# Kernel tuning notes

Measured on AMD Instinct MI355X. Metric: run time of the kernel, lower is better.

Reference implementation:

```python
import jax, jax.numpy as jnp
import numpy as np

B, R, S, D = 8, 128, 512, 33      # batch, ref (grid), seq_len, input_dim (enc_in*2+1)
E, H = 128, 4                     # embed_time, num_heads
EK = E // H                       # per-head dim
NH = 128                          # nhidden
NEG = -1e9


def setup_inputs() -> dict:
    key = jax.random.key(0)
    ks = jax.random.split(key, 16)
    inp = {
        'query': jax.random.normal(ks[0], (B, R, E), jnp.float32),
        'key':   jax.random.normal(ks[1], (B, S, E), jnp.float32),
        'value': jax.random.normal(ks[2], (B, S, D), jnp.float32),
        'mask':  (jax.random.uniform(ks[3], (B, S, D)) < 0.7).astype(jnp.float32),
        'qt':    jnp.sort(jax.random.uniform(ks[4], (R,), jnp.float32)),
        'tt':    jax.random.uniform(ks[5], (B, S), jnp.float32),
        'stride': 0.1 * jax.random.normal(ks[6], (D,), jnp.float32),
        # learned params (torch Linear layout: W [out, in])
        'Wq': jax.random.normal(ks[7], (E, E), jnp.float32) / np.sqrt(E),
        'bq': jnp.zeros((E,), jnp.float32),
        'Wk': jax.random.normal(ks[8], (E, E), jnp.float32) / np.sqrt(E),
        'bk': jnp.zeros((E,), jnp.float32),
        'Wr': jax.random.normal(ks[9], (D, D), jnp.float32) / np.sqrt(D),
        'br': jnp.zeros((D,), jnp.float32),
        'Wo': jax.random.normal(ks[10], (NH, H * D), jnp.float32) / np.sqrt(H * D),
        'bo': jnp.zeros((NH,), jnp.float32),
    }
    return inp


def reference(query, key, value, mask, qt, tt, stride, Wq, bq, Wk, bk, Wr, br, Wo, bo):
    b, r, _ = query.shape
    s = key.shape[1]
    d = value.shape[-1]
    # stride gate: sigmoid(Linear(D,D)(stride))  -> [D]
    sa = jax.nn.sigmoid(stride @ Wr.T + br)
    # projections, split heads: [B,H,R,EK] / [B,H,S,EK]
    q = (query @ Wq.T + bq).reshape(b, r, H, EK).transpose(0, 2, 1, 3)
    k = (key @ Wk.T + bk).reshape(b, s, H, EK).transpose(0, 2, 1, 3)
    # scores: [B,H,R,S]
    scores = jnp.einsum('bhre,bhse->bhrs', q, k) / np.sqrt(EK)
    # per-query time window mask, vectorized over the 'ref' loop: [B,R,S,D]
    t = tt[:, None, :, None]                      # [B,1,S,1]
    qtb = qt[None, :, None, None]                 # [1,R,1,1]
    win = (t <= qtb + sa) & (t >= qtb - sa)       # [B,R,S,D] (sa broadcasts on D)
    allm = win & (mask[:, None, :, :] != 0)       # [B,R,S,D]
    # broadcast scores over value dim D, mask, softmax over seq axis (dim=-2)
    sc = jnp.where(allm[:, None], scores[..., None], NEG)  # [B,H,R,S,D]
    p = jax.nn.softmax(sc, axis=-2)
    # masked weighted sum over seq: [B,H,R,D]
    x = jnp.einsum('bhrsd,bsd->bhrd', p, value)
    x = x.transpose(0, 2, 1, 3).reshape(b, r, H * d)
    out = x @ Wo.T + bo                           # [B,R,NH]
    return out, sa
```

## Files before the change

kernel.cpp:

```cpp
#include <hip/hip_runtime.h>

#define BB   8
#define RR   128
#define SS   512
#define DD   33
#define EE   128
#define HH   4
#define EKK  32
#define NHH  128
#define HD   (HH*DD)

#define WS_QP   0
#define WS_KT   (BB*RR*EE)
#define WS_WOT  (WS_KT + BB*EE*SS)

#define NB_KP   512
#define NB_QP2  128
#define NB_WOT2 66
#define NB_PREP (NB_KP + NB_QP2 + NB_WOT2)

__global__ __launch_bounds__(256) void prep_kernel(
    const float* __restrict__ query, const float* __restrict__ key,
    const float* __restrict__ Wq, const float* __restrict__ bq,
    const float* __restrict__ Wk, const float* __restrict__ bk,
    const float* __restrict__ Wo, float* __restrict__ ws)
{
    __shared__ float rows[8 * EE];
    int blk = blockIdx.x, tid = threadIdx.x;

    if (blk < NB_KP) {
        int s8 = blk * 8;
#pragma unroll
        for (int i = 0; i < 4; ++i) rows[i * 256 + tid] = key[s8 * EE + i * 256 + tid];
        __syncthreads();
        int g = tid >> 7, e = tid & 127;
        float acc[4];
        float bv = bk[e];
#pragma unroll
        for (int p = 0; p < 4; ++p) acc[p] = bv;
        const float4* W4 = (const float4*)(Wk + e * EE);
        const float4* R4 = (const float4*)rows;
#pragma unroll
        for (int j = 0; j < EE / 4; ++j) {
            float4 w = W4[j];
#pragma unroll
            for (int p = 0; p < 4; ++p) {
                float4 rv = R4[(g * 4 + p) * 32 + j];
                acc[p] += w.x * rv.x + w.y * rv.y + w.z * rv.z + w.w * rv.w;
            }
        }
        int b = s8 / SS, s0 = s8 % SS;
        float4 v; v.x = acc[0]; v.y = acc[1]; v.z = acc[2]; v.w = acc[3];
        *(float4*)(ws + WS_KT + (b * EE + e) * SS + s0 + g * 4) = v;
        return;
    }
    blk -= NB_KP;

    if (blk < NB_QP2) {
        int br0 = blk * 8;
#pragma unroll
        for (int i = 0; i < 4; ++i) rows[i * 256 + tid] = query[br0 * EE + i * 256 + tid];
        __syncthreads();
        int g = tid >> 7, e = tid & 127;
        float acc[4];
        float bv = bq[e];
#pragma unroll
        for (int p = 0; p < 4; ++p) acc[p] = bv;
        const float4* W4 = (const float4*)(Wq + e * EE);
        const float4* R4 = (const float4*)rows;
#pragma unroll
        for (int j = 0; j < EE / 4; ++j) {
            float4 w = W4[j];
#pragma unroll
            for (int p = 0; p < 4; ++p) {
                float4 rv = R4[(g * 4 + p) * 32 + j];
                acc[p] += w.x * rv.x + w.y * rv.y + w.z * rv.z + w.w * rv.w;
            }
        }
#pragma unroll
        for (int p = 0; p < 4; ++p)
            ws[WS_QP + (br0 + g * 4 + p) * EE + e] = acc[p];
        return;
    }
    blk -= NB_QP2;

    {
        int gid = blk * 256 + tid;
        if (gid < HD * NHH) {
            int n = gid & 127, j = gid >> 7;
            ws[WS_WOT + gid] = Wo[n * HD + j];
        }
    }
}

#define POOL_REDP 0
#define POOL_REDW 2048
#define POOL_REDV 4096
#define POOL_R32P 4352
#define POOL_R32W 4416
#define POOL_R32V 4480
#define EIDX(rr,h,s) (((rr)*HH+(h))*SS + (s))

__global__ __launch_bounds__(512) void fused_kernel(
    const float* __restrict__ qp, const float* __restrict__ kt,
    const float* __restrict__ value, const float* __restrict__ maskp,
    const float* __restrict__ tt, const float* __restrict__ qt,
    const float* __restrict__ stridev, const float* __restrict__ Wr,
    const float* __restrict__ brv, const float* __restrict__ wot,
    const float* __restrict__ bo, float* __restrict__ out)
{
    __shared__ float s_q[2][EE];
    __shared__ float s_tt[SS];
    __shared__ float s_sa[DD + 3];
    __shared__ float s_pool[4488];
    __shared__ float s_x[2][HD];
    __shared__ float s_part[4][NHH];

    int blk = blockIdx.x;
    int b  = blk >> 6;
    int r0 = (blk & 63) * 2;
    int tid = threadIdx.x;

    if (tid < 256) s_q[tid >> 7][tid & 127] =
        qp[(b * RR + r0 + (tid >> 7)) * EE + (tid & 127)];
    s_tt[tid] = tt[b * SS + tid];
    if (tid < DD) {
        float acc = brv[tid];
#pragma unroll
        for (int j = 0; j < DD; ++j) acc += stridev[j] * Wr[tid * DD + j];
        float sv = 1.0f / (1.0f + __expf(-acc));
        s_sa[tid] = sv;
        if (blk == 0) out[BB * RR * NHH + tid] = sv;
    }
    __syncthreads();

    {
        int h = tid >> 7, sq = tid & 127;
        const float* kb = kt + (b * EE + h * EKK) * SS;
        float4 a0 = {0,0,0,0}, a1 = {0,0,0,0};
#pragma unroll
        for (int e = 0; e < EKK; ++e) {
            float4 kv = ((const float4*)(kb + e * SS))[sq];
            float q0 = s_q[0][h * EKK + e];
            float q1 = s_q[1][h * EKK + e];
            a0.x += q0 * kv.x; a0.y += q0 * kv.y; a0.z += q0 * kv.z; a0.w += q0 * kv.w;
            a1.x += q1 * kv.x; a1.y += q1 * kv.y; a1.z += q1 * kv.z; a1.w += q1 * kv.w;
        }
        const float scale = 0.17677669529663687f;
        float4 e0, e1;
        e0.x = __expf(a0.x * scale); e0.y = __expf(a0.y * scale);
        e0.z = __expf(a0.z * scale); e0.w = __expf(a0.w * scale);
        e1.x = __expf(a1.x * scale); e1.y = __expf(a1.y * scale);
        e1.z = __expf(a1.z * scale); e1.w = __expf(a1.w * scale);
        ((float4*)&s_pool[EIDX(0, h, 0)])[sq] = e0;
        ((float4*)&s_pool[EIDX(1, h, 0)])[sq] = e1;
    }
    __syncthreads();

    int wv = tid >> 6, lane = tid & 63;
    int sp = lane >> 5, d = lane & 31;
    int s0 = wv * 64;
    float qtr0 = qt[r0], qtr1 = qt[r0 + 1];

    float ps0[HH] = {0,0,0,0}, ps1[HH] = {0,0,0,0};
    float ws0_[HH] = {0,0,0,0}, ws1_[HH] = {0,0,0,0};
    float vsum = 0.f;
    {
        float sad = s_sa[d];
        float lo0 = qtr0 - sad, hi0 = qtr0 + sad;
        float lo1 = qtr1 - sad, hi1 = qtr1 + sad;
        const float* vp = value + (size_t)(b * SS + s0 + sp) * DD + d;
        const float* mp = maskp + (size_t)(b * SS + s0 + sp) * DD + d;
#pragma unroll 4
        for (int i = 0; i < 32; ++i) {
            int s = s0 + 2 * i + sp;
            float vv = vp[i * 2 * DD];
            float mv = mp[i * 2 * DD];
            float tv = s_tt[s];
            bool mb = (mv != 0.f);
            bool k0 = mb & (tv >= lo0) & (tv <= hi0);
            bool k1 = mb & (tv >= lo1) & (tv <= hi1);
            vsum += vv;
#pragma unroll
            for (int h = 0; h < HH; ++h) {
                float e0 = s_pool[EIDX(0, h, s)];
                float e1 = s_pool[EIDX(1, h, s)];
                float p0 = k0 ? e0 : 0.f;
                float p1 = k1 ? e1 : 0.f;
                ps0[h] += p0; ws0_[h] += p0 * vv;
                ps1[h] += p1; ws1_[h] += p1 * vv;
            }
        }
#pragma unroll
        for (int h = 0; h < HH; ++h) {
            ps0[h] += __shfl_xor(ps0[h], 32); ws0_[h] += __shfl_xor(ws0_[h], 32);
            ps1[h] += __shfl_xor(ps1[h], 32); ws1_[h] += __shfl_xor(ws1_[h], 32);
        }
        vsum += __shfl_xor(vsum, 32);
    }

    float tps = 0.f, tws = 0.f, tvs = 0.f;
    {
        int trr = lane >> 5, th = (lane >> 3) & 3, tj = lane & 7;
        float sad = s_sa[32];
        float lo = (trr ? qtr1 : qtr0) - sad, hi = (trr ? qtr1 : qtr0) + sad;
#pragma unroll
        for (int i = 0; i < 8; ++i) {
            int s = s0 + tj * 8 + i;
            float vv = value[(size_t)(b * SS + s) * DD + 32];
            float mv = maskp[(size_t)(b * SS + s) * DD + 32];
            float tv = s_tt[s];
            bool k = (mv != 0.f) & (tv >= lo) & (tv <= hi);
            float e = s_pool[EIDX(trr, th, s)];
            float p = k ? e : 0.f;
            tps += p; tws += p * vv; tvs += vv;
        }
#pragma unroll
        for (int off = 1; off < 8; off <<= 1) {
            tps += __shfl_xor(tps, off);
            tws += __shfl_xor(tws, off);
            tvs += __shfl_xor(tvs, off);
        }
    }
    __syncthreads();

    if (lane < 32) {
#pragma unroll
        for (int h = 0; h < HH; ++h) {
            s_pool[POOL_REDP + ((wv * 2 + 0) * HH + h) * 32 + lane] = ps0[h];
            s_pool[POOL_REDP + ((wv * 2 + 1) * HH + h) * 32 + lane] = ps1[h];
            s_pool[POOL_REDW + ((wv * 2 + 0) * HH + h) * 32 + lane] = ws0_[h];
            s_pool[POOL_REDW + ((wv * 2 + 1) * HH + h) * 32 + lane] = ws1_[h];
        }
        s_pool[POOL_REDV + wv * 32 + lane] = vsum;
    }
    if ((lane & 7) == 0) {
        int trr = lane >> 5, th = (lane >> 3) & 3;
        s_pool[POOL_R32P + (wv * 2 + trr) * HH + th] = tps;
        s_pool[POOL_R32W + (wv * 2 + trr) * HH + th] = tws;
        if (lane == 0) s_pool[POOL_R32V + wv] = tvs;
    }
    __syncthreads();

    if (tid < 256) {
        int rr = tid >> 7, hd = tid & 127, h = hd >> 5, dd = hd & 31;
        float p = 0.f, w = 0.f;
#pragma unroll
        for (int k = 0; k < 8; ++k) {
            p += s_pool[POOL_REDP + ((k * 2 + rr) * HH + h) * 32 + dd];
            w += s_pool[POOL_REDW + ((k * 2 + rr) * HH + h) * 32 + dd];
        }
        float xv;
        if (p > 0.f) xv = w / p;
        else {
            float va = 0.f;
#pragma unroll
            for (int k = 0; k < 8; ++k) va += s_pool[POOL_REDV + k * 32 + dd];
            xv = va * (1.0f / SS);
        }
        s_x[rr][h * DD + dd] = xv;
    } else if (tid < 264) {
        int t = tid - 256, rr = t >> 2, h = t & 3;
        float p = 0.f, w = 0.f;
#pragma unroll
        for (int k = 0; k < 8; ++k) {
            p += s_pool[POOL_R32P + (k * 2 + rr) * HH + h];
            w += s_pool[POOL_R32W + (k * 2 + rr) * HH + h];
        }
        float xv;
        if (p > 0.f) xv = w / p;
        else {
            float va = 0.f;
#pragma unroll
            for (int k = 0; k < 8; ++k) va += s_pool[POOL_R32V + k];
            xv = va * (1.0f / SS);
        }
        s_x[rr][h * DD + 32] = xv;
    }
    __syncthreads();

    {
        int g2 = tid >> 7;
        int rr = g2 >> 1, jg = g2 & 1;
        int n = tid & 127;
        float acc = 0.f;
#pragma unroll
        for (int j = 0; j < 66; ++j)
            acc += s_x[rr][jg * 66 + j] * wot[(jg * 66 + j) * NHH + n];
        s_part[g2][n] = acc;
    }
    __syncthreads();
    if (tid < 256) {
        int rr = tid >> 7, n = tid & 127;
        out[(b * RR + r0 + rr) * NHH + n] =
            bo[n] + s_part[rr * 2][n] + s_part[rr * 2 + 1][n];
    }
}

extern "C" void kernel_launch(void* const* d_in, const int* in_sizes, int n_in,
                              void* d_out, int out_size, void* d_ws, size_t ws_size,
                              hipStream_t stream) {
    const float* query   = (const float*)d_in[0];
    const float* key     = (const float*)d_in[1];
    const float* value   = (const float*)d_in[2];
    const float* mask    = (const float*)d_in[3];
    const float* qt      = (const float*)d_in[4];
    const float* tt      = (const float*)d_in[5];
    const float* stridev = (const float*)d_in[6];
    const float* Wq      = (const float*)d_in[7];
    const float* bq      = (const float*)d_in[8];
    const float* Wk      = (const float*)d_in[9];
    const float* bk      = (const float*)d_in[10];
    const float* Wr      = (const float*)d_in[11];
    const float* brv     = (const float*)d_in[12];
    const float* Wo      = (const float*)d_in[13];
    const float* bo      = (const float*)d_in[14];

    float* out = (float*)d_out;
    float* ws  = (float*)d_ws;

    prep_kernel<<<NB_PREP, 256, 0, stream>>>(
        query, key, Wq, bq, Wk, bk, Wo, ws);
    fused_kernel<<<BB * 64, 512, 0, stream>>>(
        ws + WS_QP, ws + WS_KT, value, mask, tt, qt,
        stridev, Wr, brv, ws + WS_WOT, bo, out);
}
```

Before: 39.89 us.

## Merge prep and attention kernels into one cooperative kernel with grid sync

Folds the key projection, query projection and Wo transpose into the main attention kernel and separates them from the attention phase with a cooperative grid-wide barrier, falling back to the two-kernel path when co-residency is not possible. The query projection is now computed per block directly into shared memory instead of round-tripping through the workspace. The aim is to remove the second launch and the gap between kernels. In exchange it adds grid-sync cost, host-side occupancy queries on every call, and a co-residency requirement for 512 blocks of 512 threads.

Result: no change. 39.79 us (-0.2%).

```diff
diff --git a/kernel.cpp b/kernel.cpp
--- a/kernel.cpp
+++ b/kernel.cpp
@@ -1,4 +1,7 @@
 #include <hip/hip_runtime.h>
+#include <hip/hip_cooperative_groups.h>
+
+namespace cg = cooperative_groups;
 
 #define BB   8
 #define RR   128
@@ -10,88 +13,9 @@
 #define NHH  128
 #define HD   (HH*DD)
 
-#define WS_QP   0
-#define WS_KT   (BB*RR*EE)
-#define WS_WOT  (WS_KT + BB*EE*SS)
-
-#define NB_KP   512
-#define NB_QP2  128
-#define NB_WOT2 66
-#define NB_PREP (NB_KP + NB_QP2 + NB_WOT2)
-
-__global__ __launch_bounds__(256) void prep_kernel(
-    const float* __restrict__ query, const float* __restrict__ key,
-    const float* __restrict__ Wq, const float* __restrict__ bq,
-    const float* __restrict__ Wk, const float* __restrict__ bk,
-    const float* __restrict__ Wo, float* __restrict__ ws)
-{
-    __shared__ float rows[8 * EE];
-    int blk = blockIdx.x, tid = threadIdx.x;
-
-    if (blk < NB_KP) {
-        int s8 = blk * 8;
-#pragma unroll
-        for (int i = 0; i < 4; ++i) rows[i * 256 + tid] = key[s8 * EE + i * 256 + tid];
-        __syncthreads();
-        int g = tid >> 7, e = tid & 127;
-        float acc[4];
-        float bv = bk[e];
-#pragma unroll
-        for (int p = 0; p < 4; ++p) acc[p] = bv;
-        const float4* W4 = (const float4*)(Wk + e * EE);
-        const float4* R4 = (const float4*)rows;
-#pragma unroll
-        for (int j = 0; j < EE / 4; ++j) {
-            float4 w = W4[j];
-#pragma unroll
-            for (int p = 0; p < 4; ++p) {
-                float4 rv = R4[(g * 4 + p) * 32 + j];
-                acc[p] += w.x * rv.x + w.y * rv.y + w.z * rv.z + w.w * rv.w;
-            }
-        }
-        int b = s8 / SS, s0 = s8 % SS;
-        float4 v; v.x = acc[0]; v.y = acc[1]; v.z = acc[2]; v.w = acc[3];
-        *(float4*)(ws + WS_KT + (b * EE + e) * SS + s0 + g * 4) = v;
-        return;
-    }
-    blk -= NB_KP;
-
-    if (blk < NB_QP2) {
-        int br0 = blk * 8;
-#pragma unroll
-        for (int i = 0; i < 4; ++i) rows[i * 256 + tid] = query[br0 * EE + i * 256 + tid];
-        __syncthreads();
-        int g = tid >> 7, e = tid & 127;
-        float acc[4];
-        float bv = bq[e];
-#pragma unroll
-        for (int p = 0; p < 4; ++p) acc[p] = bv;
-        const float4* W4 = (const float4*)(Wq + e * EE);
-        const float4* R4 = (const float4*)rows;
-#pragma unroll
-        for (int j = 0; j < EE / 4; ++j) {
-            float4 w = W4[j];
-#pragma unroll
-            for (int p = 0; p < 4; ++p) {
-                float4 rv = R4[(g * 4 + p) * 32 + j];
-                acc[p] += w.x * rv.x + w.y * rv.y + w.z * rv.z + w.w * rv.w;
-            }
-        }
-#pragma unroll
-        for (int p = 0; p < 4; ++p)
-            ws[WS_QP + (br0 + g * 4 + p) * EE + e] = acc[p];
-        return;
-    }
-    blk -= NB_QP2;
-
-    {
-        int gid = blk * 256 + tid;
-        if (gid < HD * NHH) {
-            int n = gid & 127, j = gid >> 7;
-            ws[WS_WOT + gid] = Wo[n * HD + j];
-        }
-    }
-}
+#define WS_KT   0
+#define WS_WOT  (BB*EE*SS)
+#define WS_QP   (WS_WOT + HD*NHH)
 
 #define POOL_REDP 0
 #define POOL_REDW 2048
@@ -101,13 +25,16 @@
 #define POOL_R32V 4480
 #define EIDX(rr,h,s) (((rr)*HH+(h))*SS + (s))
 
-__global__ __launch_bounds__(512) void fused_kernel(
-    const float* __restrict__ qp, const float* __restrict__ kt,
+__global__ __launch_bounds__(512, 4) void mega_kernel(
+    const float* __restrict__ query, const float* __restrict__ key,
     const float* __restrict__ value, const float* __restrict__ maskp,
-    const float* __restrict__ tt, const float* __restrict__ qt,
-    const float* __restrict__ stridev, const float* __restrict__ Wr,
-    const float* __restrict__ brv, const float* __restrict__ wot,
-    const float* __restrict__ bo, float* __restrict__ out)
+    const float* __restrict__ qt, const float* __restrict__ tt,
+    const float* __restrict__ stridev,
+    const float* __restrict__ Wq, const float* __restrict__ bq,
+    const float* __restrict__ Wk, const float* __restrict__ bk,
+    const float* __restrict__ Wr, const float* __restrict__ brv,
+    const float* __restrict__ Wo, const float* __restrict__ bo,
+    float* __restrict__ ws, float* __restrict__ out)
 {
     __shared__ float s_q[2][EE];
     __shared__ float s_tt[SS];
@@ -115,14 +42,15 @@
     __shared__ float s_pool[4488];
     __shared__ float s_x[2][HD];
     __shared__ float s_part[4][NHH];
-
-    int blk = blockIdx.x;
-    int b  = blk >> 6;
-    int r0 = (blk & 63) * 2;
-    int tid = threadIdx.x;
-
-    if (tid < 256) s_q[tid >> 7][tid & 127] =
-        qp[(b * RR + r0 + (tid >> 7)) * EE + (tid & 127)];
+    __shared__ float s_rows[8 * EE];
+
+    int bid = blockIdx.x, tid = threadIdx.x;
+    int b  = bid >> 6;
+    int r0 = (bid & 63) * 2;
+
+    int s8 = bid * 8;
+    s_rows[tid]       = key[s8 * EE + tid];
+    s_rows[tid + 512] = key[s8 * EE + 512 + tid];
     s_tt[tid] = tt[b * SS + tid];
     if (tid < DD) {
         float acc = brv[tid];
@@ -130,9 +58,55 @@
         for (int j = 0; j < DD; ++j) acc += stridev[j] * Wr[tid * DD + j];
         float sv = 1.0f / (1.0f + __expf(-acc));
         s_sa[tid] = sv;
-        if (blk == 0) out[BB * RR * NHH + tid] = sv;
-    }
-    __syncthreads();
+        if (bid == 0) out[BB * RR * NHH + tid] = sv;
+    }
+    if (bid < 66) {
+        int gid = bid * 256 + tid;
+        if (gid < HD * NHH) {
+            int n = gid & 127, j = gid >> 7;
+            ws[WS_WOT + gid] = Wo[n * HD + j];
+        }
+    }
+    __syncthreads();
+
+    {
+        int g = tid >> 7, e = tid & 127;
+        float acc0 = bk[e], acc1 = acc0;
+        const float4* W4 = (const float4*)(Wk + e * EE);
+        const float4* R4 = (const float4*)s_rows;
+#pragma unroll
+        for (int j = 0; j < EE / 4; ++j) {
+            float4 w  = W4[j];
+            float4 r0v = R4[(g * 2 + 0) * 32 + j];
+            float4 r1v = R4[(g * 2 + 1) * 32 + j];
+            acc0 += w.x * r0v.x + w.y * r0v.y + w.z * r0v.z + w.w * r0v.w;
+            acc1 += w.x * r1v.x + w.y * r1v.y + w.z * r1v.z + w.w * r1v.w;
+        }
+        int kb = s8 / SS, s0 = s8 % SS;
+        float2 v; v.x = acc0; v.y = acc1;
+        *(float2*)(ws + WS_KT + (kb * EE + e) * SS + s0 + g * 2) = v;
+    }
+    __syncthreads();
+
+    if (tid < 256) s_rows[tid] = query[(b * RR + r0 + (tid >> 7)) * EE + (tid & 127)];
+    __syncthreads();
+    if (tid < 256) {
+        int rr = tid >> 7, e = tid & 127;
+        float acc = bq[e];
+        const float4* W4 = (const float4*)(Wq + e * EE);
+        const float4* R4 = (const float4*)(s_rows + rr * EE);
+#pragma unroll
+        for (int j = 0; j < EE / 4; ++j) {
+            float4 w = W4[j]; float4 rv = R4[j];
+            acc += w.x * rv.x + w.y * rv.y + w.z * rv.z + w.w * rv.w;
+        }
+        s_q[rr][e] = acc;
+    }
+
+    cg::this_grid().sync();
+
+    const float* kt  = ws + WS_KT;
+    const float* wot = ws + WS_WOT;
 
     {
         int h = tid >> 7, sq = tid & 127;
@@ -297,13 +271,288 @@
     }
 }
 
+#define NB_KP   512
+#define NB_QP2  128
+#define NB_WOT2 66
+#define NB_PREP (NB_KP + NB_QP2 + NB_WOT2)
+
+__global__ __launch_bounds__(256) void prep_kernel(
+    const float* __restrict__ query, const float* __restrict__ key,
+    const float* __restrict__ Wq, const float* __restrict__ bq,
+    const float* __restrict__ Wk, const float* __restrict__ bk,
+    const float* __restrict__ Wo, float* __restrict__ ws)
+{
+    __shared__ float rows[8 * EE];
+    int blk = blockIdx.x, tid = threadIdx.x;
+
+    if (blk < NB_KP) {
+        int s8 = blk * 8;
+#pragma unroll
+        for (int i = 0; i < 4; ++i) rows[i * 256 + tid] = key[s8 * EE + i * 256 + tid];
+        __syncthreads();
+        int g = tid >> 7, e = tid & 127;
+        float acc[4];
+        float bv = bk[e];
+#pragma unroll
+        for (int p = 0; p < 4; ++p) acc[p] = bv;
+        const float4* W4 = (const float4*)(Wk + e * EE);
+        const float4* R4 = (const float4*)rows;
+#pragma unroll
+        for (int j = 0; j < EE / 4; ++j) {
+            float4 w = W4[j];
+#pragma unroll
+            for (int p = 0; p < 4; ++p) {
+                float4 rv = R4[(g * 4 + p) * 32 + j];
+                acc[p] += w.x * rv.x + w.y * rv.y + w.z * rv.z + w.w * rv.w;
+            }
+        }
+        int b = s8 / SS, s0 = s8 % SS;
+        float4 v; v.x = acc[0]; v.y = acc[1]; v.z = acc[2]; v.w = acc[3];
+        *(float4*)(ws + WS_KT + (b * EE + e) * SS + s0 + g * 4) = v;
+        return;
+    }
+    blk -= NB_KP;
+
+    if (blk < NB_QP2) {
+        int br0 = blk * 8;
+#pragma unroll
+        for (int i = 0; i < 4; ++i) rows[i * 256 + tid] = query[br0 * EE + i * 256 + tid];
+        __syncthreads();
+        int g = tid >> 7, e = tid & 127;
+        float acc[4];
+        float bv = bq[e];
+#pragma unroll
+        for (int p = 0; p < 4; ++p) acc[p] = bv;
+        const float4* W4 = (const float4*)(Wq + e * EE);
+        const float4* R4 = (const float4*)rows;
+#pragma unroll
+        for (int j = 0; j < EE / 4; ++j) {
+            float4 w = W4[j];
+#pragma unroll
+            for (int p = 0; p < 4; ++p) {
+                float4 rv = R4[(g * 4 + p) * 32 + j];
+                acc[p] += w.x * rv.x + w.y * rv.y + w.z * rv.z + w.w * rv.w;
+            }
+        }
+#pragma unroll
+        for (int p = 0; p < 4; ++p)
+            ws[WS_QP + (br0 + g * 4 + p) * EE + e] = acc[p];
+        return;
+    }
+    blk -= NB_QP2;
+
+    {
+        int gid = blk * 256 + tid;
+        if (gid < HD * NHH) {
+            int n = gid & 127, j = gid >> 7;
+            ws[WS_WOT + gid] = Wo[n * HD + j];
+        }
+    }
+}
+
+__global__ __launch_bounds__(512) void fused_kernel(
+    const float* __restrict__ qp, const float* __restrict__ kt,
+    const float* __restrict__ value, const float* __restrict__ maskp,
+    const float* __restrict__ tt, const float* __restrict__ qt,
+    const float* __restrict__ stridev, const float* __restrict__ Wr,
+    const float* __restrict__ brv, const float* __restrict__ wot,
+    const float* __restrict__ bo, float* __restrict__ out)
+{
+    __shared__ float s_q[2][EE];
+    __shared__ float s_tt[SS];
+    __shared__ float s_sa[DD + 3];
+    __shared__ float s_pool[4488];
+    __shared__ float s_x[2][HD];
+    __shared__ float s_part[4][NHH];
+
+    int blk = blockIdx.x;
+    int b  = blk >> 6;
+    int r0 = (blk & 63) * 2;
+    int tid = threadIdx.x;
+
+    if (tid < 256) s_q[tid >> 7][tid & 127] =
+        qp[(b * RR + r0 + (tid >> 7)) * EE + (tid & 127)];
+    s_tt[tid] = tt[b * SS + tid];
+    if (tid < DD) {
+        float acc = brv[tid];
+#pragma unroll
+        for (int j = 0; j < DD; ++j) acc += stridev[j] * Wr[tid * DD + j];
+        float sv = 1.0f / (1.0f + __expf(-acc));
+        s_sa[tid] = sv;
+        if (blk == 0) out[BB * RR * NHH + tid] = sv;
+    }
+    __syncthreads();
+
+    {
+        int h = tid >> 7, sq = tid & 127;
+        const float* kb = kt + (b * EE + h * EKK) * SS;
+        float4 a0 = {0,0,0,0}, a1 = {0,0,0,0};
+#pragma unroll
+        for (int e = 0; e < EKK; ++e) {
+            float4 kv = ((const float4*)(kb + e * SS))[sq];
+            float q0 = s_q[0][h * EKK + e];
+            float q1 = s_q[1][h * EKK + e];
+            a0.x += q0 * kv.x; a0.y += q0 * kv.y; a0.z += q0 * kv.z; a0.w += q0 * kv.w;
+            a1.x += q1 * kv.x; a1.y += q1 * kv.y; a1.z += q1 * kv.z; a1.w += q1 * kv.w;
+        }
+        const float scale = 0.17677669529663687f;
+        float4 e0, e1;
+        e0.x = __expf(a0.x * scale); e0.y = __expf(a0.y * scale);
+        e0.z = __expf(a0.z * scale); e0.w = __expf(a0.w * scale);
+        e1.x = __expf(a1.x * scale); e1.y = __expf(a1.y * scale);
+        e1.z = __expf(a1.z * scale); e1.w = __expf(a1.w * scale);
+        ((float4*)&s_pool[EIDX(0, h, 0)])[sq] = e0;
+        ((float4*)&s_pool[EIDX(1, h, 0)])[sq] = e1;
+    }
+    __syncthreads();
+
+    int wv = tid >> 6, lane = tid & 63;
+    int sp = lane >> 5, d = lane & 31;
+    int s0 = wv * 64;
+    float qtr0 = qt[r0], qtr1 = qt[r0 + 1];
+
+    float ps0[HH] = {0,0,0,0}, ps1[HH] = {0,0,0,0};
+    float ws0_[HH] = {0,0,0,0}, ws1_[HH] = {0,0,0,0};
+    float vsum = 0.f;
+    {
+        float sad = s_sa[d];
+        float lo0 = qtr0 - sad, hi0 = qtr0 + sad;
+        float lo1 = qtr1 - sad, hi1 = qtr1 + sad;
+        const float* vp = value + (size_t)(b * SS + s0 + sp) * DD + d;
+        const float* mp = maskp + (size_t)(b * SS + s0 + sp) * DD + d;
+#pragma unroll 4
+        for (int i = 0; i < 32; ++i) {
+            int s = s0 + 2 * i + sp;
+            float vv = vp[i * 2 * DD];
+            float mv = mp[i * 2 * DD];
+            float tv = s_tt[s];
+            bool mb = (mv != 0.f);
+            bool k0 = mb & (tv >= lo0) & (tv <= hi0);
+            bool k1 = mb & (tv >= lo1) & (tv <= hi1);
+            vsum += vv;
+#pragma unroll
+            for (int h = 0; h < HH; ++h) {
+                float e0 = s_pool[EIDX(0, h, s)];
+                float e1 = s_pool[EIDX(1, h, s)];
+                float p0 = k0 ? e0 : 0.f;
+                float p1 = k1 ? e1 : 0.f;
+                ps0[h] += p0; ws0_[h] += p0 * vv;
+                ps1[h] += p1; ws1_[h] += p1 * vv;
+            }
+        }
+#pragma unroll
+        for (int h = 0; h < HH; ++h) {
+            ps0[h] += __shfl_xor(ps0[h], 32); ws0_[h] += __shfl_xor(ws0_[h], 32);
+            ps1[h] += __shfl_xor(ps1[h], 32); ws1_[h] += __shfl_xor(ws1_[h], 32);
+        }
+        vsum += __shfl_xor(vsum, 32);
+    }
+
+    float tps = 0.f, tws = 0.f, tvs = 0.f;
+    {
+        int trr = lane >> 5, th = (lane >> 3) & 3, tj = lane & 7;
+        float sad = s_sa[32];
+        float lo = (trr ? qtr1 : qtr0) - sad, hi = (trr ? qtr1 : qtr0) + sad;
+#pragma unroll
+        for (int i = 0; i < 8; ++i) {
+            int s = s0 + tj * 8 + i;
+            float vv = value[(size_t)(b * SS + s) * DD + 32];
+            float mv = maskp[(size_t)(b * SS + s) * DD + 32];
+            float tv = s_tt[s];
+            bool k = (mv != 0.f) & (tv >= lo) & (tv <= hi);
+            float e = s_pool[EIDX(trr, th, s)];
+            float p = k ? e : 0.f;
+            tps += p; tws += p * vv; tvs += vv;
+        }
+#pragma unroll
+        for (int off = 1; off < 8; off <<= 1) {
+            tps += __shfl_xor(tps, off);
+            tws += __shfl_xor(tws, off);
+            tvs += __shfl_xor(tvs, off);
+        }
+    }
+    __syncthreads();
+
+    if (lane < 32) {
+#pragma unroll
+        for (int h = 0; h < HH; ++h) {
+            s_pool[POOL_REDP + ((wv * 2 + 0) * HH + h) * 32 + lane] = ps0[h];
+            s_pool[POOL_REDP + ((wv * 2 + 1) * HH + h) * 32 + lane] = ps1[h];
+            s_pool[POOL_REDW + ((wv * 2 + 0) * HH + h) * 32 + lane] = ws0_[h];
+            s_pool[POOL_REDW + ((wv * 2 + 1) * HH + h) * 32 + lane] = ws1_[h];
+        }
+        s_pool[POOL_REDV + wv * 32 + lane] = vsum;
+    }
+    if ((lane & 7) == 0) {
+        int trr = lane >> 5, th = (lane >> 3) & 3;
+        s_pool[POOL_R32P + (wv * 2 + trr) * HH + th] = tps;
+        s_pool[POOL_R32W + (wv * 2 + trr) * HH + th] = tws;
+        if (lane == 0) s_pool[POOL_R32V + wv] = tvs;
+    }
+    __syncthreads();
+
+    if (tid < 256) {
+        int rr = tid >> 7, hd = tid & 127, h = hd >> 5, dd = hd & 31;
+        float p = 0.f, w = 0.f;
+#pragma unroll
+        for (int k = 0; k < 8; ++k) {
+            p += s_pool[POOL_REDP + ((k * 2 + rr) * HH + h) * 32 + dd];
+            w += s_pool[POOL_REDW + ((k * 2 + rr) * HH + h) * 32 + dd];
+        }
+        float xv;
+        if (p > 0.f) xv = w / p;
+        else {
+            float va = 0.f;
+#pragma unroll
+            for (int k = 0; k < 8; ++k) va += s_pool[POOL_REDV + k * 32 + dd];
+            xv = va * (1.0f / SS);
+        }
+        s_x[rr][h * DD + dd] = xv;
+    } else if (tid < 264) {
+        int t = tid - 256, rr = t >> 2, h = t & 3;
+        float p = 0.f, w = 0.f;
+#pragma unroll
+        for (int k = 0; k < 8; ++k) {
+            p += s_pool[POOL_R32P + (k * 2 + rr) * HH + h];
+            w += s_pool[POOL_R32W + (k * 2 + rr) * HH + h];
+        }
+        float xv;
+        if (p > 0.f) xv = w / p;
+        else {
+            float va = 0.f;
+#pragma unroll
+            for (int k = 0; k < 8; ++k) va += s_pool[POOL_R32V + k];
+            xv = va * (1.0f / SS);
+        }
+        s_x[rr][h * DD + 32] = xv;
+    }
+    __syncthreads();
+
+    {
+        int g2 = tid >> 7;
+        int rr = g2 >> 1, jg = g2 & 1;
+        int n = tid & 127;
+        float acc = 0.f;
+#pragma unroll
+        for (int j = 0; j < 66; ++j)
+            acc += s_x[rr][jg * 66 + j] * wot[(jg * 66 + j) * NHH + n];
+        s_part[g2][n] = acc;
+    }
+    __syncthreads();
+    if (tid < 256) {
+        int rr = tid >> 7, n = tid & 127;
+        out[(b * RR + r0 + rr) * NHH + n] =
+            bo[n] + s_part[rr * 2][n] + s_part[rr * 2 + 1][n];
+    }
+}
+
 extern "C" void kernel_launch(void* const* d_in, const int* in_sizes, int n_in,
                               void* d_out, int out_size, void* d_ws, size_t ws_size,
                               hipStream_t stream) {
     const float* query   = (const float*)d_in[0];
     const float* key     = (const float*)d_in[1];
     const float* value   = (const float*)d_in[2];
-    const float* mask    = (const float*)d_in[3];
+    const float* maskp   = (const float*)d_in[3];
     const float* qt      = (const float*)d_in[4];
     const float* tt      = (const float*)d_in[5];
     const float* stridev = (const float*)d_in[6];
@@ -319,9 +568,25 @@
     float* out = (float*)d_out;
     float* ws  = (float*)d_ws;
 
-    prep_kernel<<<NB_PREP, 256, 0, stream>>>(
-        query, key, Wq, bq, Wk, bk, Wo, ws);
-    fused_kernel<<<BB * 64, 512, 0, stream>>>(
-        ws + WS_QP, ws + WS_KT, value, mask, tt, qt,
-        stridev, Wr, brv, ws + WS_WOT, bo, out);
+    int dev = 0, numCU = 0, maxb = 0;
+    hipGetDevice(&dev);
+    hipDeviceGetAttribute(&numCU, hipDeviceAttributeMultiprocessorCount, dev);
+    hipOccupancyMaxActiveBlocksPerMultiprocessor(&maxb, mega_kernel, 512, 0);
+
+    if (maxb > 0 && numCU > 0 && (long)maxb * numCU >= BB * 64) {
+        void* args[] = {
+            (void*)&query, (void*)&key, (void*)&value, (void*)&maskp,
+            (void*)&qt, (void*)&tt, (void*)&stridev,
+            (void*)&Wq, (void*)&bq, (void*)&Wk, (void*)&bk,
+            (void*)&Wr, (void*)&brv, (void*)&Wo, (void*)&bo,
+            (void*)&ws, (void*)&out };
+        hipLaunchCooperativeKernel(mega_kernel, dim3(BB * 64), dim3(512),
+                                   args, 0, stream);
+    } else {
+        prep_kernel<<<NB_PREP, 256, 0, stream>>>(
+            query, key, Wq, bq, Wk, bk, Wo, ws);
+        fused_kernel<<<BB * 64, 512, 0, stream>>>(
+            ws + WS_QP, ws + WS_KT, value, maskp, tt, qt,
+            stridev, Wr, brv, ws + WS_WOT, bo, out);
+    }
 }
```

## Process one query row per block instead of two to double grid size

Applied to the files above, without the earlier changes.

The fused kernel now assigns a single ref row per 512-thread block, launching B*R blocks instead of B*R/2. Per-block shared memory and registers shrink, and launch bounds request 8 blocks per CU to raise occupancy. The cost is that each block re-reads K, value, mask and Wo for only one row, roughly doubling global and L2 traffic per output. The workspace layout is also reordered.

Result: slower. 44.87 us (+12.5%).

```diff
diff --git a/kernel.cpp b/kernel.cpp
--- a/kernel.cpp
+++ b/kernel.cpp
@@ -10,9 +10,9 @@
 #define NHH  128
 #define HD   (HH*DD)
 
-#define WS_QP   0
-#define WS_KT   (BB*RR*EE)
-#define WS_WOT  (WS_KT + BB*EE*SS)
+#define WS_KT   0
+#define WS_WOT  (BB*EE*SS)
+#define WS_QP   (WS_WOT + HD*NHH)
 
 #define NB_KP   512
 #define NB_QP2  128
@@ -93,15 +93,7 @@
     }
 }
 
-#define POOL_REDP 0
-#define POOL_REDW 2048
-#define POOL_REDV 4096
-#define POOL_R32P 4352
-#define POOL_R32W 4416
-#define POOL_R32V 4480
-#define EIDX(rr,h,s) (((rr)*HH+(h))*SS + (s))
-
-__global__ __launch_bounds__(512) void fused_kernel(
+__global__ __launch_bounds__(512, 8) void fused_kernel(
     const float* __restrict__ qp, const float* __restrict__ kt,
     const float* __restrict__ value, const float* __restrict__ maskp,
     const float* __restrict__ tt, const float* __restrict__ qt,
@@ -109,20 +101,23 @@
     const float* __restrict__ brv, const float* __restrict__ wot,
     const float* __restrict__ bo, float* __restrict__ out)
 {
-    __shared__ float s_q[2][EE];
+    __shared__ float s_q[EE];
     __shared__ float s_tt[SS];
     __shared__ float s_sa[DD + 3];
-    __shared__ float s_pool[4488];
-    __shared__ float s_x[2][HD];
+    __shared__ float s_e[HH][SS];
+    __shared__ float s_redp[8 * HH * 32];
+    __shared__ float s_redw[8 * HH * 32];
+    __shared__ float s_redv[8 * 32];
+    __shared__ float s_r32p[8 * HH];
+    __shared__ float s_r32w[8 * HH];
+    __shared__ float s_r32v[8];
+    __shared__ float s_x[HD];
     __shared__ float s_part[4][NHH];
 
-    int blk = blockIdx.x;
-    int b  = blk >> 6;
-    int r0 = (blk & 63) * 2;
-    int tid = threadIdx.x;
-
-    if (tid < 256) s_q[tid >> 7][tid & 127] =
-        qp[(b * RR + r0 + (tid >> 7)) * EE + (tid & 127)];
+    int blk = blockIdx.x, tid = threadIdx.x;
+    int b = blk >> 7, r = blk & 127;
+
+    if (tid < EE) s_q[tid] = qp[(b * RR + r) * EE + tid];
     s_tt[tid] = tt[b * SS + tid];
     if (tid < DD) {
         float acc = brv[tid];
@@ -137,38 +132,38 @@
     {
         int h = tid >> 7, sq = tid & 127;
         const float* kb = kt + (b * EE + h * EKK) * SS;
-        float4 a0 = {0,0,0,0}, a1 = {0,0,0,0};
-#pragma unroll
-        for (int e = 0; e < EKK; ++e) {
-            float4 kv = ((const float4*)(kb + e * SS))[sq];
-            float q0 = s_q[0][h * EKK + e];
-            float q1 = s_q[1][h * EKK + e];
-            a0.x += q0 * kv.x; a0.y += q0 * kv.y; a0.z += q0 * kv.z; a0.w += q0 * kv.w;
-            a1.x += q1 * kv.x; a1.y += q1 * kv.y; a1.z += q1 * kv.z; a1.w += q1 * kv.w;
+        const float4* q4p = (const float4*)(s_q + h * EKK);
+        float4 a = {0.f, 0.f, 0.f, 0.f};
+#pragma unroll
+        for (int e4 = 0; e4 < 8; ++e4) {
+            float4 q4 = q4p[e4];
+            float4 k0 = ((const float4*)(kb + (e4 * 4 + 0) * SS))[sq];
+            float4 k1 = ((const float4*)(kb + (e4 * 4 + 1) * SS))[sq];
+            float4 k2 = ((const float4*)(kb + (e4 * 4 + 2) * SS))[sq];
+            float4 k3 = ((const float4*)(kb + (e4 * 4 + 3) * SS))[sq];
+            a.x += q4.x * k0.x + q4.y * k1.x + q4.z * k2.x + q4.w * k3.x;
+            a.y += q4.x * k0.y + q4.y * k1.y + q4.z * k2.y + q4.w * k3.y;
+            a.z += q4.x * k0.z + q4.y * k1.z + q4.z * k2.z + q4.w * k3.z;
+            a.w += q4.x * k0.w + q4.y * k1.w + q4.z * k2.w + q4.w * k3.w;
         }
         const float scale = 0.17677669529663687f;
-        float4 e0, e1;
-        e0.x = __expf(a0.x * scale); e0.y = __expf(a0.y * scale);
-        e0.z = __expf(a0.z * scale); e0.w = __expf(a0.w * scale);
-        e1.x = __expf(a1.x * scale); e1.y = __expf(a1.y * scale);
-        e1.z = __expf(a1.z * scale); e1.w = __expf(a1.w * scale);
-        ((float4*)&s_pool[EIDX(0, h, 0)])[sq] = e0;
-        ((float4*)&s_pool[EIDX(1, h, 0)])[sq] = e1;
+        float4 ev;
+        ev.x = __expf(a.x * scale); ev.y = __expf(a.y * scale);
+        ev.z = __expf(a.z * scale); ev.w = __expf(a.w * scale);
+        ((float4*)s_e[h])[sq] = ev;
     }
     __syncthreads();
 
     int wv = tid >> 6, lane = tid & 63;
     int sp = lane >> 5, d = lane & 31;
     int s0 = wv * 64;
-    float qtr0 = qt[r0], qtr1 = qt[r0 + 1];
-
-    float ps0[HH] = {0,0,0,0}, ps1[HH] = {0,0,0,0};
-    float ws0_[HH] = {0,0,0,0}, ws1_[HH] = {0,0,0,0};
+    float qtr = qt[r];
+
+    float ps[HH] = {0,0,0,0}, wsum[HH] = {0,0,0,0};
     float vsum = 0.f;
     {
         float sad = s_sa[d];
-        float lo0 = qtr0 - sad, hi0 = qtr0 + sad;
-        float lo1 = qtr1 - sad, hi1 = qtr1 + sad;
+        float lo = qtr - sad, hi = qtr + sad;
         const float* vp = value + (size_t)(b * SS + s0 + sp) * DD + d;
         const float* mp = maskp + (size_t)(b * SS + s0 + sp) * DD + d;
 #pragma unroll 4
@@ -177,124 +172,112 @@
             float vv = vp[i * 2 * DD];
             float mv = mp[i * 2 * DD];
             float tv = s_tt[s];
-            bool mb = (mv != 0.f);
-            bool k0 = mb & (tv >= lo0) & (tv <= hi0);
-            bool k1 = mb & (tv >= lo1) & (tv <= hi1);
+            bool k = (mv != 0.f) & (tv >= lo) & (tv <= hi);
             vsum += vv;
 #pragma unroll
             for (int h = 0; h < HH; ++h) {
-                float e0 = s_pool[EIDX(0, h, s)];
-                float e1 = s_pool[EIDX(1, h, s)];
-                float p0 = k0 ? e0 : 0.f;
-                float p1 = k1 ? e1 : 0.f;
-                ps0[h] += p0; ws0_[h] += p0 * vv;
-                ps1[h] += p1; ws1_[h] += p1 * vv;
+                float e = s_e[h][s];
+                float p = k ? e : 0.f;
+                ps[h] += p; wsum[h] += p * vv;
             }
         }
 #pragma unroll
         for (int h = 0; h < HH; ++h) {
-            ps0[h] += __shfl_xor(ps0[h], 32); ws0_[h] += __shfl_xor(ws0_[h], 32);
-            ps1[h] += __shfl_xor(ps1[h], 32); ws1_[h] += __shfl_xor(ws1_[h], 32);
+            ps[h]   += __shfl_xor(ps[h],   32);
+            wsum[h] += __shfl_xor(wsum[h], 32);
         }
         vsum += __shfl_xor(vsum, 32);
     }
 
     float tps = 0.f, tws = 0.f, tvs = 0.f;
     {
-        int trr = lane >> 5, th = (lane >> 3) & 3, tj = lane & 7;
+        int th = lane >> 4, tj = lane & 15;
         float sad = s_sa[32];
-        float lo = (trr ? qtr1 : qtr0) - sad, hi = (trr ? qtr1 : qtr0) + sad;
-#pragma unroll
-        for (int i = 0; i < 8; ++i) {
-            int s = s0 + tj * 8 + i;
+        float lo = qtr - sad, hi = qtr + sad;
+#pragma unroll
+        for (int i = 0; i < 4; ++i) {
+            int s = s0 + tj * 4 + i;
             float vv = value[(size_t)(b * SS + s) * DD + 32];
             float mv = maskp[(size_t)(b * SS + s) * DD + 32];
             float tv = s_tt[s];
             bool k = (mv != 0.f) & (tv >= lo) & (tv <= hi);
-            float e = s_pool[EIDX(trr, th, s)];
+            float e = s_e[th][s];
             float p = k ? e : 0.f;
             tps += p; tws += p * vv; tvs += vv;
         }
 #pragma unroll
-        for (int off = 1; off < 8; off <<= 1) {
+        for (int off = 1; off < 16; off <<= 1) {
             tps += __shfl_xor(tps, off);
             tws += __shfl_xor(tws, off);
             tvs += __shfl_xor(tvs, off);
         }
     }
-    __syncthreads();
 
     if (lane < 32) {
 #pragma unroll
         for (int h = 0; h < HH; ++h) {
-            s_pool[POOL_REDP + ((wv * 2 + 0) * HH + h) * 32 + lane] = ps0[h];
-            s_pool[POOL_REDP + ((wv * 2 + 1) * HH + h) * 32 + lane] = ps1[h];
-            s_pool[POOL_REDW + ((wv * 2 + 0) * HH + h) * 32 + lane] = ws0_[h];
-            s_pool[POOL_REDW + ((wv * 2 + 1) * HH + h) * 32 + lane] = ws1_[h];
-        }
-        s_pool[POOL_REDV + wv * 32 + lane] = vsum;
-    }
-    if ((lane & 7) == 0) {
-        int trr = lane >> 5, th = (lane >> 3) & 3;
-        s_pool[POOL_R32P + (wv * 2 + trr) * HH + th] = tps;
-        s_pool[POOL_R32W + (wv * 2 + trr) * HH + th] = tws;
-        if (lane == 0) s_pool[POOL_R32V + wv] = tvs;
-    }
-    __syncthreads();
-
-    if (tid < 256) {
-        int rr = tid >> 7, hd = tid & 127, h = hd >> 5, dd = hd & 31;
+            s_redp[(wv * HH + h) * 32 + d] = ps[h];
+            s_redw[(wv * HH + h) * 32 + d] = wsum[h];
+        }
+        s_redv[wv * 32 + d] = vsum;
+    }
+    if ((lane & 15) == 0) {
+        int th = lane >> 4;
+        s_r32p[wv * HH + th] = tps;
+        s_r32w[wv * HH + th] = tws;
+        if (lane == 0) s_r32v[wv] = tvs;
+    }
+    __syncthreads();
+
+    if (tid < 128) {
+        int h = tid >> 5, dd = tid & 31;
         float p = 0.f, w = 0.f;
 #pragma unroll
         for (int k = 0; k < 8; ++k) {
-            p += s_pool[POOL_REDP + ((k * 2 + rr) * HH + h) * 32 + dd];
-            w += s_pool[POOL_REDW + ((k * 2 + rr) * HH + h) * 32 + dd];
+            p += s_redp[(k * HH + h) * 32 + dd];
+            w += s_redw[(k * HH + h) * 32 + dd];
         }
         float xv;
         if (p > 0.f) xv = w / p;
         else {
             float va = 0.f;
 #pragma unroll
-            for (int k = 0; k < 8; ++k) va += s_pool[POOL_REDV + k * 32 + dd];
+            for (int k = 0; k < 8; ++k) va += s_redv[k * 32 + dd];
             xv = va * (1.0f / SS);
         }
-        s_x[rr][h * DD + dd] = xv;
-    } else if (tid < 264) {
-        int t = tid - 256, rr = t >> 2, h = t & 3;
+        s_x[h * DD + dd] = xv;
+    } else if (tid < 132) {
+        int h = tid - 128;
         float p = 0.f, w = 0.f;
 #pragma unroll
         for (int k = 0; k < 8; ++k) {
-            p += s_pool[POOL_R32P + (k * 2 + rr) * HH + h];
-            w += s_pool[POOL_R32W + (k * 2 + rr) * HH + h];
+            p += s_r32p[k * HH + h];
+            w += s_r32w[k * HH + h];
         }
         float xv;
         if (p > 0.f) xv = w / p;
         else {
             float va = 0.f;
 #pragma unroll
-            for (int k = 0; k < 8; ++k) va += s_pool[POOL_R32V + k];
+            for (int k = 0; k < 8; ++k) va += s_r32v[k];
             xv = va * (1.0f / SS);
         }
-        s_x[rr][h * DD + 32] = xv;
-    }
-    __syncthreads();
-
-    {
-        int g2 = tid >> 7;
-        int rr = g2 >> 1, jg = g2 & 1;
-        int n = tid & 127;
+        s_x[h * DD + 32] = xv;
+    }
+    __syncthreads();
+
+    {
+        int g = tid >> 7, n = tid & 127;
         float acc = 0.f;
 #pragma unroll
-        for (int j = 0; j < 66; ++j)
-            acc += s_x[rr][jg * 66 + j] * wot[(jg * 66 + j) * NHH + n];
-        s_part[g2][n] = acc;
-    }
-    __syncthreads();
-    if (tid < 256) {
-        int rr = tid >> 7, n = tid & 127;
-        out[(b * RR + r0 + rr) * NHH + n] =
-            bo[n] + s_part[rr * 2][n] + s_part[rr * 2 + 1][n];
-    }
+        for (int j = 0; j < 33; ++j)
+            acc += s_x[g * 33 + j] * wot[(g * 33 + j) * NHH + n];
+        s_part[g][n] = acc;
+    }
+    __syncthreads();
+    if (tid < NHH)
+        out[(b * RR + r) * NHH + tid] = bo[tid] + s_part[0][tid] + s_part[1][tid]
+                                      + s_part[2][tid] + s_part[3][tid];
 }
 
 extern "C" void kernel_launch(void* const* d_in, const int* in_sizes, int n_in,
@@ -303,7 +286,7 @@
     const float* query   = (const float*)d_in[0];
     const float* key     = (const float*)d_in[1];
     const float* value   = (const float*)d_in[2];
-    const float* mask    = (const float*)d_in[3];
+    const float* maskp   = (const float*)d_in[3];
     const float* qt      = (const float*)d_in[4];
     const float* tt      = (const float*)d_in[5];
     const float* stridev = (const float*)d_in[6];
@@ -321,7 +304,7 @@
 
     prep_kernel<<<NB_PREP, 256, 0, stream>>>(
         query, key, Wq, bq, Wk, bk, Wo, ws);
-    fused_kernel<<<BB * 64, 512, 0, stream>>>(
-        ws + WS_QP, ws + WS_KT, value, mask, tt, qt,
+    fused_kernel<<<BB * RR, 512, 0, stream>>>(
+        ws + WS_QP, ws + WS_KT, value, maskp, tt, qt,
         stridev, Wr, brv, ws + WS_WOT, bo, out);
 }
```

## Transpose value to seq-major and pack mask into bitmask in prep kernel

Applied to the files above, without the earlier changes.

The prep kernel gains 64 blocks. Each transposes a strip of value into a [B,D,S] layout in the workspace and packs the float mask into 32-bit words, one bit per sequence position. The fused kernel then reads value with contiguous float4 loads, pulls mask bits from shared memory, and vectorises the score and exp reads from the shared pool. The QK inner loop also loads q in float4 groups. This targets the strided, redundant value and mask reads that every attention block repeats, at the cost of extra prep work and workspace traffic.

Result: slower. 42.99 us (+7.8%).

```diff
diff --git a/kernel.cpp b/kernel.cpp
--- a/kernel.cpp
+++ b/kernel.cpp
@@ -10,25 +10,30 @@
 #define NHH  128
 #define HD   (HH*DD)
 
-#define WS_QP   0
-#define WS_KT   (BB*RR*EE)
-#define WS_WOT  (WS_KT + BB*EE*SS)
+#define WS_KT   0
+#define WS_WOT  (BB*EE*SS)
+#define WS_QP   (WS_WOT + HD*NHH)
+#define WS_VT   (WS_QP + BB*RR*EE)
+#define WS_MB   (WS_VT + BB*DD*SS)
 
 #define NB_KP   512
 #define NB_QP2  128
 #define NB_WOT2 66
-#define NB_PREP (NB_KP + NB_QP2 + NB_WOT2)
+#define NB_VM   64
+#define NB_PREP (NB_KP + NB_QP2 + NB_WOT2 + NB_VM)
 
 __global__ __launch_bounds__(256) void prep_kernel(
     const float* __restrict__ query, const float* __restrict__ key,
+    const float* __restrict__ value, const float* __restrict__ maskp,
     const float* __restrict__ Wq, const float* __restrict__ bq,
     const float* __restrict__ Wk, const float* __restrict__ bk,
     const float* __restrict__ Wo, float* __restrict__ ws)
 {
-    __shared__ float rows[8 * EE];
+    __shared__ float s_mem[4352];
     int blk = blockIdx.x, tid = threadIdx.x;
 
     if (blk < NB_KP) {
+        float* rows = s_mem;
         int s8 = blk * 8;
 #pragma unroll
         for (int i = 0; i < 4; ++i) rows[i * 256 + tid] = key[s8 * EE + i * 256 + tid];
@@ -57,6 +62,7 @@
     blk -= NB_KP;
 
     if (blk < NB_QP2) {
+        float* rows = s_mem;
         int br0 = blk * 8;
 #pragma unroll
         for (int i = 0; i < 4; ++i) rows[i * 256 + tid] = query[br0 * EE + i * 256 + tid];
@@ -84,11 +90,39 @@
     }
     blk -= NB_QP2;
 
-    {
+    if (blk < NB_WOT2) {
         int gid = blk * 256 + tid;
         if (gid < HD * NHH) {
             int n = gid & 127, j = gid >> 7;
             ws[WS_WOT + gid] = Wo[n * HD + j];
+        }
+        return;
+    }
+    blk -= NB_WOT2;
+
+    {
+        float* tile_v = s_mem;
+        float* tile_m = s_mem + 2176;
+        int b = blk >> 3, strip = blk & 7;
+        int s0 = strip * 64;
+        int flat = (b * SS + s0) * DD;
+        for (int i = tid; i < 64 * DD; i += 256) {
+            int s = i / DD, d = i - s * DD;
+            tile_v[d * 65 + s] = value[flat + i];
+            tile_m[d * 65 + s] = maskp[flat + i];
+        }
+        __syncthreads();
+        for (int i = tid; i < DD * 64; i += 256) {
+            int d = i >> 6, s = i & 63;
+            ws[WS_VT + (b * DD + d) * SS + s0 + s] = tile_v[d * 65 + s];
+        }
+        if (tid < 2 * DD) {
+            int wl = tid / DD, d = tid - wl * DD;
+            unsigned bits = 0;
+#pragma unroll
+            for (int j = 0; j < 32; ++j)
+                if (tile_m[d * 65 + wl * 32 + j] != 0.f) bits |= (1u << j);
+            ((unsigned*)(ws + WS_MB))[(b * 16 + strip * 2 + wl) * 36 + d] = bits;
         }
     }
 }
@@ -103,7 +137,7 @@
 
 __global__ __launch_bounds__(512) void fused_kernel(
     const float* __restrict__ qp, const float* __restrict__ kt,
-    const float* __restrict__ value, const float* __restrict__ maskp,
+    const float* __restrict__ vt, const unsigned* __restrict__ mb,
     const float* __restrict__ tt, const float* __restrict__ qt,
     const float* __restrict__ stridev, const float* __restrict__ Wr,
     const float* __restrict__ brv, const float* __restrict__ wot,
@@ -112,18 +146,19 @@
     __shared__ float s_q[2][EE];
     __shared__ float s_tt[SS];
     __shared__ float s_sa[DD + 3];
+    __shared__ unsigned s_mb[16 * 36];
     __shared__ float s_pool[4488];
     __shared__ float s_x[2][HD];
     __shared__ float s_part[4][NHH];
 
-    int blk = blockIdx.x;
+    int blk = blockIdx.x, tid = threadIdx.x;
     int b  = blk >> 6;
     int r0 = (blk & 63) * 2;
-    int tid = threadIdx.x;
 
     if (tid < 256) s_q[tid >> 7][tid & 127] =
         qp[(b * RR + r0 + (tid >> 7)) * EE + (tid & 127)];
     s_tt[tid] = tt[b * SS + tid];
+    for (int i = tid; i < 16 * 36; i += 512) s_mb[i] = mb[b * 16 * 36 + i];
     if (tid < DD) {
         float acc = brv[tid];
 #pragma unroll
@@ -137,14 +172,24 @@
     {
         int h = tid >> 7, sq = tid & 127;
         const float* kb = kt + (b * EE + h * EKK) * SS;
+        const float4* q40 = (const float4*)(&s_q[0][h * EKK]);
+        const float4* q41 = (const float4*)(&s_q[1][h * EKK]);
         float4 a0 = {0,0,0,0}, a1 = {0,0,0,0};
 #pragma unroll
-        for (int e = 0; e < EKK; ++e) {
-            float4 kv = ((const float4*)(kb + e * SS))[sq];
-            float q0 = s_q[0][h * EKK + e];
-            float q1 = s_q[1][h * EKK + e];
-            a0.x += q0 * kv.x; a0.y += q0 * kv.y; a0.z += q0 * kv.z; a0.w += q0 * kv.w;
-            a1.x += q1 * kv.x; a1.y += q1 * kv.y; a1.z += q1 * kv.z; a1.w += q1 * kv.w;
+        for (int e4 = 0; e4 < 8; ++e4) {
+            float4 qa = q40[e4], qb = q41[e4];
+            float4 k0 = ((const float4*)(kb + (e4 * 4 + 0) * SS))[sq];
+            float4 k1 = ((const float4*)(kb + (e4 * 4 + 1) * SS))[sq];
+            float4 k2 = ((const float4*)(kb + (e4 * 4 + 2) * SS))[sq];
+            float4 k3 = ((const float4*)(kb + (e4 * 4 + 3) * SS))[sq];
+            a0.x += qa.x*k0.x + qa.y*k1.x + qa.z*k2.x + qa.w*k3.x;
+            a0.y += qa.x*k0.y + qa.y*k1.y + qa.z*k2.y + qa.w*k3.y;
+            a0.z += qa.x*k0.z + qa.y*k1.z + qa.z*k2.z + qa.w*k3.z;
+            a0.w += qa.x*k0.w + qa.y*k1.w + qa.z*k2.w + qa.w*k3.w;
+            a1.x += qb.x*k0.x + qb.y*k1.x + qb.z*k2.x + qb.w*k3.x;
+            a1.y += qb.x*k0.y + qb.y*k1.y + qb.z*k2.y + qb.w*k3.y;
+            a1.z += qb.x*k0.z + qb.y*k1.z + qb.z*k2.z + qb.w*k3.z;
+            a1.w += qb.x*k0.w + qb.y*k1.w + qb.z*k2.w + qb.w*k3.w;
         }
         const float scale = 0.17677669529663687f;
         float4 e0, e1;
@@ -152,8 +197,8 @@
         e0.z = __expf(a0.z * scale); e0.w = __expf(a0.w * scale);
         e1.x = __expf(a1.x * scale); e1.y = __expf(a1.y * scale);
         e1.z = __expf(a1.z * scale); e1.w = __expf(a1.w * scale);
-        ((float4*)&s_pool[EIDX(0, h, 0)])[sq] = e0;
-        ((float4*)&s_pool[EIDX(1, h, 0)])[sq] = e1;
+        *(float4*)&s_pool[EIDX(0, h, 4 * sq)] = e0;
+        *(float4*)&s_pool[EIDX(1, h, 4 * sq)] = e1;
     }
     __syncthreads();
 
@@ -169,26 +214,38 @@
         float sad = s_sa[d];
         float lo0 = qtr0 - sad, hi0 = qtr0 + sad;
         float lo1 = qtr1 - sad, hi1 = qtr1 + sad;
-        const float* vp = value + (size_t)(b * SS + s0 + sp) * DD + d;
-        const float* mp = maskp + (size_t)(b * SS + s0 + sp) * DD + d;
-#pragma unroll 4
-        for (int i = 0; i < 32; ++i) {
-            int s = s0 + 2 * i + sp;
-            float vv = vp[i * 2 * DD];
-            float mv = mp[i * 2 * DD];
-            float tv = s_tt[s];
-            bool mb = (mv != 0.f);
-            bool k0 = mb & (tv >= lo0) & (tv <= hi0);
-            bool k1 = mb & (tv >= lo1) & (tv <= hi1);
-            vsum += vv;
+        const float* vrow = vt + (b * DD + d) * SS;
+#pragma unroll
+        for (int i = 0; i < 8; ++i) {
+            int s4 = s0 + i * 8 + sp * 4;
+            float4 vv4 = *(const float4*)(vrow + s4);
+            float4 t4  = *(const float4*)(s_tt + s4);
+            unsigned mw = s_mb[(s4 >> 5) * 36 + d];
+            unsigned mnib = (mw >> (s4 & 31)) & 0xFu;
+            float4 e0h[HH], e1h[HH];
 #pragma unroll
             for (int h = 0; h < HH; ++h) {
-                float e0 = s_pool[EIDX(0, h, s)];
-                float e1 = s_pool[EIDX(1, h, s)];
-                float p0 = k0 ? e0 : 0.f;
-                float p1 = k1 ? e1 : 0.f;
-                ps0[h] += p0; ws0_[h] += p0 * vv;
-                ps1[h] += p1; ws1_[h] += p1 * vv;
+                e0h[h] = *(const float4*)&s_pool[EIDX(0, h, s4)];
+                e1h[h] = *(const float4*)&s_pool[EIDX(1, h, s4)];
+            }
+            float tvs4[4] = {t4.x, t4.y, t4.z, t4.w};
+            float vvs4[4] = {vv4.x, vv4.y, vv4.z, vv4.w};
+#pragma unroll
+            for (int u = 0; u < 4; ++u) {
+                float tv = tvs4[u], vv = vvs4[u];
+                bool mbit = (mnib >> u) & 1u;
+                bool k0 = mbit & (tv >= lo0) & (tv <= hi0);
+                bool k1 = mbit & (tv >= lo1) & (tv <= hi1);
+                vsum += vv;
+#pragma unroll
+                for (int h = 0; h < HH; ++h) {
+                    float e0v = ((const float*)&e0h[h])[u];
+                    float e1v = ((const float*)&e1h[h])[u];
+                    float p0 = k0 ? e0v : 0.f;
+                    float p1 = k1 ? e1v : 0.f;
+                    ps0[h] += p0; ws0_[h] = fmaf(p0, vv, ws0_[h]);
+                    ps1[h] += p1; ws1_[h] = fmaf(p1, vv, ws1_[h]);
+                }
             }
         }
 #pragma unroll
@@ -203,17 +260,26 @@
     {
         int trr = lane >> 5, th = (lane >> 3) & 3, tj = lane & 7;
         float sad = s_sa[32];
-        float lo = (trr ? qtr1 : qtr0) - sad, hi = (trr ? qtr1 : qtr0) + sad;
+        float qtrX = trr ? qtr1 : qtr0;
+        float lo = qtrX - sad, hi = qtrX + sad;
+        int sb = s0 + tj * 8;
+        const float* vrow32 = vt + (b * DD + 32) * SS;
+        float4 va = *(const float4*)(vrow32 + sb);
+        float4 vb = *(const float4*)(vrow32 + sb + 4);
+        float4 ta = *(const float4*)(s_tt + sb);
+        float4 tb = *(const float4*)(s_tt + sb + 4);
+        unsigned mw = s_mb[(sb >> 5) * 36 + 32];
+        unsigned mbyte = (mw >> (sb & 31)) & 0xFFu;
+        float4 ea = *(const float4*)&s_pool[EIDX(trr, th, sb)];
+        float4 eb = *(const float4*)&s_pool[EIDX(trr, th, sb + 4)];
+        float tvals[8] = {ta.x,ta.y,ta.z,ta.w,tb.x,tb.y,tb.z,tb.w};
+        float vvals[8] = {va.x,va.y,va.z,va.w,vb.x,vb.y,vb.z,vb.w};
+        float evals[8] = {ea.x,ea.y,ea.z,ea.w,eb.x,eb.y,eb.z,eb.w};
 #pragma unroll
         for (int i = 0; i < 8; ++i) {
-            int s = s0 + tj * 8 + i;
-            float vv = value[(size_t)(b * SS + s) * DD + 32];
-            float mv = maskp[(size_t)(b * SS + s) * DD + 32];
-            float tv = s_tt[s];
-            bool k = (mv != 0.f) & (tv >= lo) & (tv <= hi);
-            float e = s_pool[EIDX(trr, th, s)];
-            float p = k ? e : 0.f;
-            tps += p; tws += p * vv; tvs += vv;
+            bool k = ((mbyte >> i) & 1u) & (tvals[i] >= lo) & (tvals[i] <= hi);
+            float p = k ? evals[i] : 0.f;
+            tps += p; tws = fmaf(p, vvals[i], tws); tvs += vvals[i];
         }
 #pragma unroll
         for (int off = 1; off < 8; off <<= 1) {
@@ -227,12 +293,12 @@
     if (lane < 32) {
 #pragma unroll
         for (int h = 0; h < HH; ++h) {
-            s_pool[POOL_REDP + ((wv * 2 + 0) * HH + h) * 32 + lane] = ps0[h];
-            s_pool[POOL_REDP + ((wv * 2 + 1) * HH + h) * 32 + lane] = ps1[h];
-            s_pool[POOL_REDW + ((wv * 2 + 0) * HH + h) * 32 + lane] = ws0_[h];
-            s_pool[POOL_REDW + ((wv * 2 + 1) * HH + h) * 32 + lane] = ws1_[h];
-        }
-        s_pool[POOL_REDV + wv * 32 + lane] = vsum;
+            s_pool[POOL_REDP + ((wv * 2 + 0) * HH + h) * 32 + d] = ps0[h];
+            s_pool[POOL_REDP + ((wv * 2 + 1) * HH + h) * 32 + d] = ps1[h];
+            s_pool[POOL_REDW + ((wv * 2 + 0) * HH + h) * 32 + d] = ws0_[h];
+            s_pool[POOL_REDW + ((wv * 2 + 1) * HH + h) * 32 + d] = ws1_[h];
+        }
+        s_pool[POOL_REDV + wv * 32 + d] = vsum;
     }
     if ((lane & 7) == 0) {
         int trr = lane >> 5, th = (lane >> 3) & 3;
@@ -303,7 +369,7 @@
     const float* query   = (const float*)d_in[0];
     const float* key     = (const float*)d_in[1];
     const float* value   = (const float*)d_in[2];
-    const float* mask    = (const float*)d_in[3];
+    const float* maskp   = (const float*)d_in[3];
     const float* qt      = (const float*)d_in[4];
     const float* tt      = (const float*)d_in[5];
     const float* stridev = (const float*)d_in[6];
@@ -320,8 +386,8 @@
     float* ws  = (float*)d_ws;
 
     prep_kernel<<<NB_PREP, 256, 0, stream>>>(
-        query, key, Wq, bq, Wk, bk, Wo, ws);
+        query, key, value, maskp, Wq, bq, Wk, bk, Wo, ws);
     fused_kernel<<<BB * 64, 512, 0, stream>>>(
-        ws + WS_QP, ws + WS_KT, value, mask, tt, qt,
-        stridev, Wr, brv, ws + WS_WOT, bo, out);
+        ws + WS_QP, ws + WS_KT, ws + WS_VT, (const unsigned*)(ws + WS_MB),
+        tt, qt, stridev, Wr, brv, ws + WS_WOT, bo, out);
 }
```
